# Performance work log

Measured on AMD Instinct MI355X. Metric: run time of the kernel, lower is better.

## Reference

```python
import jax, jax.numpy as jnp
import numpy as np

B, N, E = 4, 8192, 1024
H, G = 16, 64            # num_heads, num_groups
D = E // H               # head_dim = 64
GS = N // G              # group (block) size = 128


def setup_inputs() -> dict:
    key = jax.random.key(0)
    ks = jax.random.split(key, 11)
    std = 0.02
    mk = lambda k, shape: (jax.random.normal(k, shape, dtype=jnp.float32) * std)
    return {
        "q": jax.random.normal(ks[0], (B, N, E), dtype=jnp.float32),
        "k": jax.random.normal(ks[1], (B, N, E), dtype=jnp.float32),
        "v": jax.random.normal(ks[2], (B, N, E), dtype=jnp.float32),
        "Wq": mk(ks[3], (E, E)), "bq": jnp.zeros((E,), jnp.float32),
        "Wk": mk(ks[4], (E, E)), "bk": jnp.zeros((E,), jnp.float32),
        "Wv": mk(ks[5], (E, E)), "bv": jnp.zeros((E,), jnp.float32),
        "Wo": mk(ks[6], (E, E)), "bo": jnp.zeros((E,), jnp.float32),
    }


def reference(q, k, v, Wq, bq, Wk, bk, Wv, bv, Wo, bo):
    b, n, e = q.shape
    scale = 1.0 / (D ** 0.5)

    def proj(x, W, bias):
        # [b,n,e] -> [b,H,G,GS,D]  (split heads, then split seq into groups)
        y = x @ W + bias
        return y.reshape(b, n, H, D).transpose(0, 2, 1, 3).reshape(b, H, G, GS, D)

    qh = proj(q, Wq, bq)
    kh = proj(k, Wk, bk)
    vh = proj(v, Wv, bv)

    # block-diagonal attention: each seq group attends only within itself
    scores = jnp.einsum('bhgqd,bhgkd->bhgqk', qh, kh) * scale  # [b,H,G,GS,GS]
    w = jax.nn.softmax(scores, axis=-1)
    og = jnp.einsum('bhgqk,bhgkd->bhgqd', w, vh)               # [b,H,G,GS,D]

    out = og.reshape(b, H, n, D).transpose(0, 2, 1, 3).reshape(b, n, e)
    out = out @ Wo + bo
    # torch version returns attn_weights of the last group from the loop
    return out, w[:, :, -1]
```

## Files before the change

### kernel.cpp

```cpp
#include <hip/hip_runtime.h>
#include <stdint.h>

#define DEVI static __device__ __forceinline__

typedef __attribute__((ext_vector_type(8))) __bf16 bf16x8;
typedef __attribute__((ext_vector_type(4))) float f32x4;

#define MFMA16(a, b, c) __builtin_amdgcn_mfma_f32_16x16x32_bf16((a), (b), (c), 0, 0, 0)

DEVI uint16_t f2bf(float f) {
  uint32_t u = __builtin_bit_cast(uint32_t, f);
  u += 0x7fffu + ((u >> 16) & 1u);
  return (uint16_t)(u >> 16);
}

DEVI void gload16(const void* g, void* l) {
  __builtin_amdgcn_global_load_lds((const __attribute__((address_space(1))) void*)g,
                                   (__attribute__((address_space(3))) void*)l, 16, 0, 0);
}

#define BARRIER()                         \
  do {                                    \
    __builtin_amdgcn_sched_barrier(0);    \
    __builtin_amdgcn_s_barrier();         \
    __builtin_amdgcn_sched_barrier(0);    \
  } while (0)

__global__ __launch_bounds__(256) void cvt_bf16(const float* __restrict__ in,
                                                uint16_t* __restrict__ out, long n) {
  long i = ((long)blockIdx.x * 256 + threadIdx.x) * 8;
  if (i >= n) return;
  float4 a = *(const float4*)(in + i);
  float4 b = *(const float4*)(in + i + 4);
  union { uint16_t u[8]; uint4 v; } r;
  r.u[0] = f2bf(a.x); r.u[1] = f2bf(a.y); r.u[2] = f2bf(a.z); r.u[3] = f2bf(a.w);
  r.u[4] = f2bf(b.x); r.u[5] = f2bf(b.y); r.u[6] = f2bf(b.z); r.u[7] = f2bf(b.w);
  *(uint4*)(out + i) = r.v;
}

struct W4 {
  const float* W[4];
  uint16_t* Wt[4];
};

__global__ __launch_bounds__(256) void wtrans4(W4 p) {
  __shared__ float t[64][65];
  const float* __restrict__ W = p.W[blockIdx.z];
  uint16_t* __restrict__ Wt = p.Wt[blockIdx.z];
  const int ti = blockIdx.y * 64, tj = blockIdx.x * 64;
  {
    int r = threadIdx.x >> 2, c0 = (threadIdx.x & 3) * 16;
#pragma unroll
    for (int i = 0; i < 16; i += 4) {
      float4 v = *(const float4*)(W + (size_t)(ti + r) * 1024 + tj + c0 + i);
      t[r][c0 + i + 0] = v.x; t[r][c0 + i + 1] = v.y;
      t[r][c0 + i + 2] = v.z; t[r][c0 + i + 3] = v.w;
    }
  }
  __syncthreads();
  {
    int c = threadIdx.x >> 2, r0 = (threadIdx.x & 3) * 16;
    union { uint16_t u[16]; uint4 v[2]; } b;
#pragma unroll
    for (int i = 0; i < 16; ++i) b.u[i] = f2bf(t[r0 + i][c]);
    uint16_t* dst = Wt + (size_t)(tj + c) * 1024 + ti + r0;
    *(uint4*)dst = b.v[0];
    *(uint4*)(dst + 8) = b.v[1];
  }
}

__global__ __launch_bounds__(512, 2) void gemm256(const uint16_t* __restrict__ A,
                                                  const uint16_t* __restrict__ Bt,
                                                  const float* __restrict__ bias,
                                                  void* __restrict__ C, int cf32) {
  __shared__ uint8_t lds[163840];
  const int tid = threadIdx.x;
  const int l = tid & 63, w = tid >> 6;
  const int wr = w >> 2, wc = w & 3;
  const int lc = l & 15, lq = l >> 4;

  const int bid = blockIdx.y * 4 + blockIdx.x;
  const int swz = (bid & 7) * 64 + (bid >> 3);
  const size_t m0 = (size_t)(swz >> 2) * 256;
  const int n0 = (swz & 3) * 256;

  const uint8_t* Ab = (const uint8_t*)A + m0 * 2048;
  const uint8_t* Bb = (const uint8_t*)Bt + (size_t)n0 * 2048;

  const int srow = tid >> 3;
  const int susw = ((tid & 7) ^ (srow & 7)) * 16;

  auto stageA = [&](int sb, int kt) {
#pragma unroll
    for (int j = 0; j < 4; ++j)
      gload16(Ab + (size_t)(j * 64 + srow) * 2048 + kt * 128 + susw,
              lds + sb * 32768 + j * 8192 + w * 1024);
  };
  auto stageB = [&](int db, int kt) {
#pragma unroll
    for (int j = 0; j < 4; ++j)
      gload16(Bb + (size_t)(j * 64 + srow) * 2048 + kt * 128 + susw,
              lds + 98304 + db * 32768 + j * 8192 + w * 1024);
  };

  auto ldsA = [&](int sb, int mi, int kk) -> bf16x8 {
    const int row = wr * 128 + mi * 16 + lc;
    const int u = ((kk * 4 + lq) ^ (row & 7)) * 16;
    return *(const bf16x8*)(lds + sb * 32768 + row * 128 + u);
  };
  auto ldsB = [&](int db, int ni, int kk) -> bf16x8 {
    const int row = wc * 64 + ni * 16 + lc;
    const int u = ((kk * 4 + lq) ^ (row & 7)) * 16;
    return *(const bf16x8*)(lds + 98304 + db * 32768 + row * 128 + u);
  };

  f32x4 acc[8][4] = {};

  stageA(0, 0);
  stageB(0, 0);
  stageA(1, 1);
  asm volatile("s_waitcnt vmcnt(4)" ::: "memory");
  BARRIER();

  for (int t = 0; t < 16; ++t) {
    const int ab = t % 3;
    const int bb = t & 1;
    if (t + 1 < 16) stageB((t + 1) & 1, t + 1);
    if (t + 2 < 16) stageA((t + 2) % 3, t + 2);

#pragma unroll
    for (int kk = 0; kk < 2; ++kk) {
      bf16x8 bF[4], aF[8];
#pragma unroll
      for (int ni = 0; ni < 4; ++ni) bF[ni] = ldsB(bb, ni, kk);
#pragma unroll
      for (int mi = 0; mi < 8; ++mi) aF[mi] = ldsA(ab, mi, kk);
      __builtin_amdgcn_s_setprio(1);
#pragma unroll
      for (int mi = 0; mi < 8; ++mi)
#pragma unroll
        for (int ni = 0; ni < 4; ++ni)
          acc[mi][ni] = MFMA16(aF[mi], bF[ni], acc[mi][ni]);
      __builtin_amdgcn_s_setprio(0);
    }

    if (t < 14)       { asm volatile("s_waitcnt vmcnt(4)" ::: "memory"); }
    else if (t == 14) { asm volatile("s_waitcnt vmcnt(0)" ::: "memory"); }
    if (t < 15) BARRIER();
  }

#pragma unroll
  for (int mi = 0; mi < 8; ++mi) {
#pragma unroll
    for (int ni = 0; ni < 4; ++ni) {
      const int col = n0 + wc * 64 + ni * 16 + lc;
      const float bb2 = bias[col];
#pragma unroll
      for (int r = 0; r < 4; ++r) {
        const size_t row = m0 + wr * 128 + mi * 16 + lq * 4 + r;
        const float vv = acc[mi][ni][r] + bb2;
        if (cf32) ((float*)C)[row * 1024 + col] = vv;
        else      ((uint16_t*)C)[row * 1024 + col] = f2bf(vv);
      }
    }
  }
}

__global__ __launch_bounds__(256) void attn(const uint16_t* __restrict__ Qh,
                                            const uint16_t* __restrict__ Kh,
                                            const uint16_t* __restrict__ Vh,
                                            uint16_t* __restrict__ Oh,
                                            float* __restrict__ Wlast) {
  __shared__ uint16_t Ks[128][72];
  __shared__ uint16_t Vt[64][136];
  __shared__ uint16_t Ps[128][136];

  const int blk = blockIdx.x;
  const int b = blk >> 10;
  const int h = (blk >> 6) & 15;
  const int g = blk & 63;
  const size_t rowbase = (size_t)b * 8192 + (size_t)g * 128;
  const int colbase = h * 64;

  const int tid = threadIdx.x, lane = tid & 63, wv = tid >> 6;
  const int lc = lane & 15, lq = lane >> 4;
  const int m0 = wv * 32;

  {
    const int r = tid >> 1, hf = (tid & 1) * 32;
    const uint16_t* ksrc = Kh + (rowbase + r) * 1024 + colbase + hf;
    const uint16_t* vsrc = Vh + (rowbase + r) * 1024 + colbase + hf;
    union { uint16_t u[32]; uint4 v[4]; } kk, vb;
#pragma unroll
    for (int i = 0; i < 4; ++i) kk.v[i] = *(const uint4*)(ksrc + i * 8);
#pragma unroll
    for (int i = 0; i < 4; ++i) vb.v[i] = *(const uint4*)(vsrc + i * 8);
#pragma unroll
    for (int i = 0; i < 4; ++i) *(uint4*)&Ks[r][hf + i * 8] = kk.v[i];
#pragma unroll
    for (int j = 0; j < 32; ++j) Vt[hf + j][r] = vb.u[j];
  }

  bf16x8 aq[2][2];
#pragma unroll
  for (int mi = 0; mi < 2; ++mi)
#pragma unroll
    for (int ks = 0; ks < 2; ++ks)
      aq[mi][ks] = *(const bf16x8*)(Qh + (rowbase + m0 + mi * 16 + lc) * 1024 +
                                    colbase + ks * 32 + lq * 8);

  __syncthreads();

  f32x4 sacc[2][8] = {};
#pragma unroll
  for (int ks = 0; ks < 2; ++ks) {
#pragma unroll
    for (int ni = 0; ni < 8; ++ni) {
      bf16x8 bk = *(const bf16x8*)&Ks[ni * 16 + lc][ks * 32 + lq * 8];
      sacc[0][ni] = MFMA16(aq[0][ks], bk, sacc[0][ni]);
      sacc[1][ni] = MFMA16(aq[1][ks], bk, sacc[1][ni]);
    }
  }

  const float scale = 0.125f;
  float mx[2][4], sm[2][4];
#pragma unroll
  for (int mi = 0; mi < 2; ++mi)
#pragma unroll
    for (int r = 0; r < 4; ++r) {
      float m = -1e30f;
#pragma unroll
      for (int ni = 0; ni < 8; ++ni) m = fmaxf(m, sacc[mi][ni][r]);
      m = fmaxf(m, __shfl_xor(m, 1));
      m = fmaxf(m, __shfl_xor(m, 2));
      m = fmaxf(m, __shfl_xor(m, 4));
      m = fmaxf(m, __shfl_xor(m, 8));
      mx[mi][r] = m * scale;
    }
#pragma unroll
  for (int mi = 0; mi < 2; ++mi)
#pragma unroll
    for (int ni = 0; ni < 8; ++ni)
#pragma unroll
      for (int r = 0; r < 4; ++r)
        sacc[mi][ni][r] = __expf(sacc[mi][ni][r] * scale - mx[mi][r]);
#pragma unroll
  for (int mi = 0; mi < 2; ++mi)
#pragma unroll
    for (int r = 0; r < 4; ++r) {
      float s = 0.f;
#pragma unroll
      for (int ni = 0; ni < 8; ++ni) s += sacc[mi][ni][r];
      s += __shfl_xor(s, 1); s += __shfl_xor(s, 2);
      s += __shfl_xor(s, 4); s += __shfl_xor(s, 8);
      sm[mi][r] = 1.0f / s;
    }

#pragma unroll
  for (int mi = 0; mi < 2; ++mi)
#pragma unroll
    for (int ni = 0; ni < 8; ++ni)
#pragma unroll
      for (int r = 0; r < 4; ++r) {
        float wgt = sacc[mi][ni][r] * sm[mi][r];
        sacc[mi][ni][r] = wgt;
        Ps[m0 + mi * 16 + lq * 4 + r][ni * 16 + lc] = f2bf(wgt);
      }
  if (g == 63) {
    float* wl = Wlast + (size_t)(b * 16 + h) * 16384;
#pragma unroll
    for (int mi = 0; mi < 2; ++mi)
#pragma unroll
      for (int ni = 0; ni < 8; ++ni)
#pragma unroll
        for (int r = 0; r < 4; ++r)
          wl[(size_t)(m0 + mi * 16 + lq * 4 + r) * 128 + ni * 16 + lc] =
              sacc[mi][ni][r];
  }
  __syncthreads();

  f32x4 oacc[2][4] = {};
#pragma unroll
  for (int ks = 0; ks < 4; ++ks) {
    bf16x8 ap[2], bq[4];
#pragma unroll
    for (int mi = 0; mi < 2; ++mi)
      ap[mi] = *(const bf16x8*)&Ps[m0 + mi * 16 + lc][ks * 32 + lq * 8];
#pragma unroll
    for (int ni = 0; ni < 4; ++ni)
      bq[ni] = *(const bf16x8*)&Vt[ni * 16 + lc][ks * 32 + lq * 8];
#pragma unroll
    for (int mi = 0; mi < 2; ++mi)
#pragma unroll
      for (int ni = 0; ni < 4; ++ni)
        oacc[mi][ni] = MFMA16(ap[mi], bq[ni], oacc[mi][ni]);
  }
#pragma unroll
  for (int mi = 0; mi < 2; ++mi)
#pragma unroll
    for (int ni = 0; ni < 4; ++ni)
#pragma unroll
      for (int r = 0; r < 4; ++r)
        Oh[(rowbase + m0 + mi * 16 + lq * 4 + r) * 1024 + colbase + ni * 16 + lc] =
            f2bf(oacc[mi][ni][r]);
}

extern "C" void kernel_launch(void* const* d_in, const int* in_sizes, int n_in,
                              void* d_out, int out_size, void* d_ws, size_t ws_size,
                              hipStream_t stream) {
  (void)in_sizes; (void)n_in; (void)out_size; (void)ws_size;
  const float* q  = (const float*)d_in[0];
  const float* k  = (const float*)d_in[1];
  const float* v  = (const float*)d_in[2];
  const float* Wq = (const float*)d_in[3];
  const float* bq = (const float*)d_in[4];
  const float* Wk = (const float*)d_in[5];
  const float* bk = (const float*)d_in[6];
  const float* Wv = (const float*)d_in[7];
  const float* bv = (const float*)d_in[8];
  const float* Wo = (const float*)d_in[9];
  const float* bo = (const float*)d_in[10];

  uint8_t* ws = (uint8_t*)d_ws;
  const size_t WSZ = (size_t)1024 * 1024 * 2;
  const size_t TSZ = (size_t)32768 * 1024 * 2;
  uint16_t* Wtq = (uint16_t*)(ws + 0 * WSZ);
  uint16_t* Wtk = (uint16_t*)(ws + 1 * WSZ);
  uint16_t* Wtv = (uint16_t*)(ws + 2 * WSZ);
  uint16_t* Wto = (uint16_t*)(ws + 3 * WSZ);
  uint16_t* Qh  = (uint16_t*)(ws + 4 * WSZ);
  uint16_t* Khp = (uint16_t*)(ws + 4 * WSZ + 1 * TSZ);
  uint16_t* Vhp = (uint16_t*)(ws + 4 * WSZ + 2 * TSZ);
  uint16_t* Xs  = (uint16_t*)(ws + 4 * WSZ + 3 * TSZ);

  W4 wt;
  wt.W[0] = Wq; wt.W[1] = Wk; wt.W[2] = Wv; wt.W[3] = Wo;
  wt.Wt[0] = Wtq; wt.Wt[1] = Wtk; wt.Wt[2] = Wtv; wt.Wt[3] = Wto;
  wtrans4<<<dim3(16, 16, 4), 256, 0, stream>>>(wt);

  const long NE = (long)32768 * 1024;
  const dim3 gg(4, 128), gb(512);
  cvt_bf16<<<16384, 256, 0, stream>>>(q, Xs, NE);
  gemm256<<<gg, gb, 0, stream>>>(Xs, Wtq, bq, Qh, 0);
  cvt_bf16<<<16384, 256, 0, stream>>>(k, Xs, NE);
  gemm256<<<gg, gb, 0, stream>>>(Xs, Wtk, bk, Khp, 0);
  cvt_bf16<<<16384, 256, 0, stream>>>(v, Xs, NE);
  gemm256<<<gg, gb, 0, stream>>>(Xs, Wtv, bv, Vhp, 0);

  float* outp = (float*)d_out;
  attn<<<4096, 256, 0, stream>>>(Qh, Khp, Vhp, Xs, outp + (size_t)32768 * 1024);
  gemm256<<<gg, gb, 0, stream>>>(Xs, Wto, bo, outp, 1);
}
```

Baseline: 473.9 us.

## Fuse fp32-to-bf16 input conversion into a batched QKV projection GEMM

Drops the three separate fp32-to-bf16 conversion kernels and has a new GEMM load fp32 activations straight into registers, convert them and write them to swizzled LDS. The Q, K and V projections are batched into one launch over grid z=3, so there are fewer launches and a larger wave of blocks. This removes one write and one read of a bf16 staging copy for each input. In exchange, the A operand goes through registers with a full vmcnt(0) wait each iteration, so the pipelining may be less deep than in the original gemm256.

```diff
diff --git a/kernel.cpp b/kernel.cpp
--- a/kernel.cpp
+++ b/kernel.cpp
@@ -25,18 +25,6 @@
     __builtin_amdgcn_s_barrier();         \
     __builtin_amdgcn_sched_barrier(0);    \
   } while (0)
-
-__global__ __launch_bounds__(256) void cvt_bf16(const float* __restrict__ in,
-                                                uint16_t* __restrict__ out, long n) {
-  long i = ((long)blockIdx.x * 256 + threadIdx.x) * 8;
-  if (i >= n) return;
-  float4 a = *(const float4*)(in + i);
-  float4 b = *(const float4*)(in + i + 4);
-  union { uint16_t u[8]; uint4 v; } r;
-  r.u[0] = f2bf(a.x); r.u[1] = f2bf(a.y); r.u[2] = f2bf(a.z); r.u[3] = f2bf(a.w);
-  r.u[4] = f2bf(b.x); r.u[5] = f2bf(b.y); r.u[6] = f2bf(b.z); r.u[7] = f2bf(b.w);
-  *(uint4*)(out + i) = r.v;
-}
 
 struct W4 {
   const float* W[4];
@@ -161,6 +149,131 @@
         const float vv = acc[mi][ni][r] + bb2;
         if (cf32) ((float*)C)[row * 1024 + col] = vv;
         else      ((uint16_t*)C)[row * 1024 + col] = f2bf(vv);
+      }
+    }
+  }
+}
+
+struct Proj3 {
+  const float* A[3];
+  const uint16_t* W[3];
+  const float* b[3];
+  uint16_t* C[3];
+};
+
+__global__ __launch_bounds__(512, 2) void gemm_proj3(Proj3 p) {
+  __shared__ uint8_t lds[131072];
+  const int tid = threadIdx.x;
+  const int l = tid & 63, w = tid >> 6;
+  const int wr = w >> 2, wc = w & 3;
+  const int lc = l & 15, lq = l >> 4;
+  const int z = blockIdx.z;
+
+  const int bid = blockIdx.y * 4 + blockIdx.x;
+  const int swz = (bid & 7) * 64 + (bid >> 3);
+  const size_t m0 = (size_t)(swz >> 2) * 256;
+  const int n0 = (swz & 3) * 256;
+
+  const float* Af = p.A[z];
+  const uint8_t* Bb = (const uint8_t*)p.W[z] + (size_t)n0 * 2048;
+  const float* bias = p.b[z];
+  uint16_t* C = p.C[z];
+
+  const int srow = tid >> 3;
+  const int susw = ((tid & 7) ^ (srow & 7)) * 16;
+  auto stageB = [&](int db, int kt) {
+#pragma unroll
+    for (int j = 0; j < 4; ++j)
+      gload16(Bb + (size_t)(j * 64 + srow) * 2048 + kt * 128 + susw,
+              lds + 65536 + db * 32768 + j * 8192 + w * 1024);
+  };
+
+  auto loadA = [&](int kt, float4 (&ra)[8]) {
+#pragma unroll
+    for (int j = 0; j < 8; ++j) {
+      const int row = w * 32 + j * 4 + (l >> 4);
+      ra[j] = *(const float4*)(Af + (m0 + row) * 1024 + kt * 64 + (l & 15) * 4);
+    }
+  };
+  auto writeA = [&](int sel, const float4 (&ra)[8]) {
+#pragma unroll
+    for (int j = 0; j < 8; ++j) {
+      const int row = w * 32 + j * 4 + (l >> 4);
+      const int u = (l & 15) >> 1;
+      union { uint16_t h[4]; uint2 v; } tv;
+      tv.h[0] = f2bf(ra[j].x); tv.h[1] = f2bf(ra[j].y);
+      tv.h[2] = f2bf(ra[j].z); tv.h[3] = f2bf(ra[j].w);
+      *(uint2*)(lds + sel * 32768 + row * 128 + ((u ^ (row & 7)) << 4) + (l & 1) * 8) = tv.v;
+    }
+  };
+
+  auto ldsA = [&](int sb, int mi, int kk) -> bf16x8 {
+    const int row = wr * 128 + mi * 16 + lc;
+    const int u = ((kk * 4 + lq) ^ (row & 7)) * 16;
+    return *(const bf16x8*)(lds + sb * 32768 + row * 128 + u);
+  };
+  auto ldsB = [&](int db, int ni, int kk) -> bf16x8 {
+    const int row = wc * 64 + ni * 16 + lc;
+    const int u = ((kk * 4 + lq) ^ (row & 7)) * 16;
+    return *(const bf16x8*)(lds + 65536 + db * 32768 + row * 128 + u);
+  };
+
+  f32x4 acc[8][4] = {};
+
+  {
+    float4 r0[8];
+    loadA(0, r0);
+    stageB(0, 0);
+    writeA(0, r0);
+    asm volatile("s_waitcnt vmcnt(0)" ::: "memory");
+    asm volatile("s_waitcnt lgkmcnt(0)" ::: "memory");
+  }
+  BARRIER();
+
+  for (int t = 0; t < 16; ++t) {
+    const int cur = t & 1;
+    const bool more = (t + 1 < 16);
+    float4 ra[8];
+    if (more) {
+      stageB(cur ^ 1, t + 1);
+      loadA(t + 1, ra);
+    }
+    __builtin_amdgcn_sched_barrier(0);
+
+#pragma unroll
+    for (int kk = 0; kk < 2; ++kk) {
+      bf16x8 bF[4], aF[8];
+#pragma unroll
+      for (int ni = 0; ni < 4; ++ni) bF[ni] = ldsB(cur, ni, kk);
+#pragma unroll
+      for (int mi = 0; mi < 8; ++mi) aF[mi] = ldsA(cur, mi, kk);
+      __builtin_amdgcn_s_setprio(1);
+#pragma unroll
+      for (int mi = 0; mi < 8; ++mi)
+#pragma unroll
+        for (int ni = 0; ni < 4; ++ni)
+          acc[mi][ni] = MFMA16(aF[mi], bF[ni], acc[mi][ni]);
+      __builtin_amdgcn_s_setprio(0);
+    }
+
+    if (more) {
+      writeA(cur ^ 1, ra);
+      asm volatile("s_waitcnt vmcnt(0)" ::: "memory");
+      asm volatile("s_waitcnt lgkmcnt(0)" ::: "memory");
+      BARRIER();
+    }
+  }
+
+#pragma unroll
+  for (int mi = 0; mi < 8; ++mi) {
+#pragma unroll
+    for (int ni = 0; ni < 4; ++ni) {
+      const int col = n0 + wc * 64 + ni * 16 + lc;
+      const float bb2 = bias[col];
+#pragma unroll
+      for (int r = 0; r < 4; ++r) {
+        const size_t row = m0 + wr * 128 + mi * 16 + lq * 4 + r;
+        C[row * 1024 + col] = f2bf(acc[mi][ni][r] + bb2);
       }
     }
   }
@@ -338,16 +451,14 @@
   wt.Wt[0] = Wtq; wt.Wt[1] = Wtk; wt.Wt[2] = Wtv; wt.Wt[3] = Wto;
   wtrans4<<<dim3(16, 16, 4), 256, 0, stream>>>(wt);
 
-  const long NE = (long)32768 * 1024;
-  const dim3 gg(4, 128), gb(512);
-  cvt_bf16<<<16384, 256, 0, stream>>>(q, Xs, NE);
-  gemm256<<<gg, gb, 0, stream>>>(Xs, Wtq, bq, Qh, 0);
-  cvt_bf16<<<16384, 256, 0, stream>>>(k, Xs, NE);
-  gemm256<<<gg, gb, 0, stream>>>(Xs, Wtk, bk, Khp, 0);
-  cvt_bf16<<<16384, 256, 0, stream>>>(v, Xs, NE);
-  gemm256<<<gg, gb, 0, stream>>>(Xs, Wtv, bv, Vhp, 0);
+  Proj3 p;
+  p.A[0] = q;  p.A[1] = k;  p.A[2] = v;
+  p.W[0] = Wtq; p.W[1] = Wtk; p.W[2] = Wtv;
+  p.b[0] = bq; p.b[1] = bk; p.b[2] = bv;
+  p.C[0] = Qh; p.C[1] = Khp; p.C[2] = Vhp;
+  gemm_proj3<<<dim3(4, 128, 3), 512, 0, stream>>>(p);
 
   float* outp = (float*)d_out;
   attn<<<4096, 256, 0, stream>>>(Qh, Khp, Vhp, Xs, outp + (size_t)32768 * 1024);
-  gemm256<<<gg, gb, 0, stream>>>(Xs, Wto, bo, outp, 1);
-}
+  gemm256<<<dim3(4, 128), 512, 0, stream>>>(Xs, Wto, bo, outp, 1);
+}
```

New measurement: 479.5 us. About the same (+1.2%).

## Split GEMM main loop into four interleaved load/MFMA phases with barriers

Applied to the files above, without the earlier changes.

Restructures the projection GEMM inner loop into four quadrant phases, each loading part of the A/B fragments from LDS and issuing half of the global-to-LDS staging before running a quarter of the MFMAs. This aims to overlap LDS reads and global prefetches with matrix math, in the style of a ping-pong schedule. In exchange it adds many workgroup barriers and lgkmcnt fences per k-step, which can serialize waves if the phases don't balance.

```diff
diff --git a/kernel.cpp b/kernel.cpp
--- a/kernel.cpp
+++ b/kernel.cpp
@@ -24,6 +24,12 @@
     __builtin_amdgcn_sched_barrier(0);    \
     __builtin_amdgcn_s_barrier();         \
     __builtin_amdgcn_sched_barrier(0);    \
+  } while (0)
+
+#define LGKM0_FENCE()                                      \
+  do {                                                     \
+    asm volatile("s_waitcnt lgkmcnt(0)" ::: "memory");     \
+    __builtin_amdgcn_sched_barrier(0);                     \
   } while (0)
 
 __global__ __launch_bounds__(256) void cvt_bf16(const float* __restrict__ in,
@@ -90,15 +96,15 @@
   const int srow = tid >> 3;
   const int susw = ((tid & 7) ^ (srow & 7)) * 16;
 
-  auto stageA = [&](int sb, int kt) {
-#pragma unroll
-    for (int j = 0; j < 4; ++j)
+  auto stageA_h = [&](int sb, int kt, int h) {
+#pragma unroll
+    for (int j = 2 * h; j < 2 * h + 2; ++j)
       gload16(Ab + (size_t)(j * 64 + srow) * 2048 + kt * 128 + susw,
               lds + sb * 32768 + j * 8192 + w * 1024);
   };
-  auto stageB = [&](int db, int kt) {
-#pragma unroll
-    for (int j = 0; j < 4; ++j)
+  auto stageB_h = [&](int db, int kt, int h) {
+#pragma unroll
+    for (int j = 2 * h; j < 2 * h + 2; ++j)
       gload16(Bb + (size_t)(j * 64 + srow) * 2048 + kt * 128 + susw,
               lds + 98304 + db * 32768 + j * 8192 + w * 1024);
   };
@@ -116,33 +122,90 @@
 
   f32x4 acc[8][4] = {};
 
-  stageA(0, 0);
-  stageB(0, 0);
-  stageA(1, 1);
+  stageA_h(0, 0, 0); stageA_h(0, 0, 1);
+  stageB_h(0, 0, 0); stageB_h(0, 0, 1);
+  stageA_h(1, 1, 0); stageA_h(1, 1, 1);
   asm volatile("s_waitcnt vmcnt(4)" ::: "memory");
   BARRIER();
 
   for (int t = 0; t < 16; ++t) {
     const int ab = t % 3;
     const int bb = t & 1;
-    if (t + 1 < 16) stageB((t + 1) & 1, t + 1);
-    if (t + 2 < 16) stageA((t + 2) % 3, t + 2);
+    const int nbB = (t + 1) & 1;
+    const int nbA = (t + 2) % 3;
+    const bool stB = (t + 1) < 16;
+    const bool stA = (t + 2) < 16;
+
+    bf16x8 aF[4][2], bF[4][2], aG[4][2];
 
 #pragma unroll
     for (int kk = 0; kk < 2; ++kk) {
-      bf16x8 bF[4], aF[8];
-#pragma unroll
-      for (int ni = 0; ni < 4; ++ni) bF[ni] = ldsB(bb, ni, kk);
-#pragma unroll
-      for (int mi = 0; mi < 8; ++mi) aF[mi] = ldsA(ab, mi, kk);
-      __builtin_amdgcn_s_setprio(1);
-#pragma unroll
-      for (int mi = 0; mi < 8; ++mi)
-#pragma unroll
-        for (int ni = 0; ni < 4; ++ni)
-          acc[mi][ni] = MFMA16(aF[mi], bF[ni], acc[mi][ni]);
-      __builtin_amdgcn_s_setprio(0);
-    }
+#pragma unroll
+      for (int mi = 0; mi < 4; ++mi) aF[mi][kk] = ldsA(ab, mi, kk);
+#pragma unroll
+      for (int ni = 0; ni < 2; ++ni) bF[ni][kk] = ldsB(bb, ni, kk);
+    }
+    if (stB) stageB_h(nbB, t + 1, 0);
+    BARRIER();
+    LGKM0_FENCE();
+    __builtin_amdgcn_s_setprio(1);
+#pragma unroll
+    for (int mi = 0; mi < 4; ++mi)
+#pragma unroll
+      for (int ni = 0; ni < 2; ++ni) {
+        acc[mi][ni] = MFMA16(aF[mi][0], bF[ni][0], acc[mi][ni]);
+        acc[mi][ni] = MFMA16(aF[mi][1], bF[ni][1], acc[mi][ni]);
+      }
+    __builtin_amdgcn_s_setprio(0);
+    BARRIER();
+
+#pragma unroll
+    for (int kk = 0; kk < 2; ++kk)
+#pragma unroll
+      for (int ni = 2; ni < 4; ++ni) bF[ni][kk] = ldsB(bb, ni, kk);
+    if (stB) stageB_h(nbB, t + 1, 1);
+    BARRIER();
+    LGKM0_FENCE();
+    __builtin_amdgcn_s_setprio(1);
+#pragma unroll
+    for (int mi = 0; mi < 4; ++mi)
+#pragma unroll
+      for (int ni = 2; ni < 4; ++ni) {
+        acc[mi][ni] = MFMA16(aF[mi][0], bF[ni][0], acc[mi][ni]);
+        acc[mi][ni] = MFMA16(aF[mi][1], bF[ni][1], acc[mi][ni]);
+      }
+    __builtin_amdgcn_s_setprio(0);
+    BARRIER();
+
+#pragma unroll
+    for (int kk = 0; kk < 2; ++kk)
+#pragma unroll
+      for (int mi = 0; mi < 4; ++mi) aG[mi][kk] = ldsA(ab, mi + 4, kk);
+    if (stA) stageA_h(nbA, t + 2, 0);
+    BARRIER();
+    LGKM0_FENCE();
+    __builtin_amdgcn_s_setprio(1);
+#pragma unroll
+    for (int mi = 0; mi < 4; ++mi)
+#pragma unroll
+      for (int ni = 0; ni < 2; ++ni) {
+        acc[mi + 4][ni] = MFMA16(aG[mi][0], bF[ni][0], acc[mi + 4][ni]);
+        acc[mi + 4][ni] = MFMA16(aG[mi][1], bF[ni][1], acc[mi + 4][ni]);
+      }
+    __builtin_amdgcn_s_setprio(0);
+    BARRIER();
+
+    if (stA) stageA_h(nbA, t + 2, 1);
+    BARRIER();
+    __builtin_amdgcn_s_setprio(1);
+#pragma unroll
+    for (int mi = 0; mi < 4; ++mi)
+#pragma unroll
+      for (int ni = 2; ni < 4; ++ni) {
+        acc[mi + 4][ni] = MFMA16(aG[mi][0], bF[ni][0], acc[mi + 4][ni]);
+        acc[mi + 4][ni] = MFMA16(aG[mi][1], bF[ni][1], acc[mi + 4][ni]);
+      }
+    __builtin_amdgcn_s_setprio(0);
 
     if (t < 14)       { asm volatile("s_waitcnt vmcnt(4)" ::: "memory"); }
     else if (t == 14) { asm volatile("s_waitcnt vmcnt(0)" ::: "memory"); }
```

After: 471.2 us. Within noise of the previous version (-0.6%).

## Replace 256x256 GEMM tile with 128x128 tile and double-buffered pipeline

Applied to the files above, without the earlier changes.

Swaps the 512-thread 256x256 GEMM (160KB LDS, triple-buffered A, double-buffered B) for a 256-thread 128x128 tile using 48KB LDS, so three blocks can share a CU. B is single-buffered: the B fragments are pulled into registers and a barrier is taken before the next tile is prefetched, while A is double-buffered. The aim is higher occupancy and more blocks to balance the wave across CUs. In exchange each tile has lower arithmetic intensity, generates more global traffic, and adds an extra barrier plus a full vmcnt(0) wait every K step.

```diff
diff --git a/kernel.cpp b/kernel.cpp
--- a/kernel.cpp
+++ b/kernel.cpp
@@ -24,6 +24,12 @@
     __builtin_amdgcn_sched_barrier(0);    \
     __builtin_amdgcn_s_barrier();         \
     __builtin_amdgcn_sched_barrier(0);    \
+  } while (0)
+
+#define LGKM0_FENCE()                                      \
+  do {                                                     \
+    asm volatile("s_waitcnt lgkmcnt(0)" ::: "memory");     \
+    __builtin_amdgcn_sched_barrier(0);                     \
   } while (0)
 
 __global__ __launch_bounds__(256) void cvt_bf16(const float* __restrict__ in,
@@ -69,96 +75,109 @@
   }
 }
 
-__global__ __launch_bounds__(512, 2) void gemm256(const uint16_t* __restrict__ A,
+__global__ __launch_bounds__(256, 3) void gemm128(const uint16_t* __restrict__ A,
                                                   const uint16_t* __restrict__ Bt,
                                                   const float* __restrict__ bias,
                                                   void* __restrict__ C, int cf32) {
-  __shared__ uint8_t lds[163840];
+  __shared__ uint8_t lds[49152];
   const int tid = threadIdx.x;
   const int l = tid & 63, w = tid >> 6;
-  const int wr = w >> 2, wc = w & 3;
+  const int wr = w >> 1, wc = w & 1;
   const int lc = l & 15, lq = l >> 4;
 
-  const int bid = blockIdx.y * 4 + blockIdx.x;
-  const int swz = (bid & 7) * 64 + (bid >> 3);
-  const size_t m0 = (size_t)(swz >> 2) * 256;
-  const int n0 = (swz & 3) * 256;
+  const int bid = blockIdx.y * 8 + blockIdx.x;
+  const int swz = (bid & 7) * 256 + (bid >> 3);
+  const size_t m0 = (size_t)(swz >> 3) * 128;
+  const int n0 = (swz & 7) * 128;
 
   const uint8_t* Ab = (const uint8_t*)A + m0 * 2048;
   const uint8_t* Bb = (const uint8_t*)Bt + (size_t)n0 * 2048;
 
-  const int srow = tid >> 3;
-  const int susw = ((tid & 7) ^ (srow & 7)) * 16;
-
-  auto stageA = [&](int sb, int kt) {
-#pragma unroll
-    for (int j = 0; j < 4; ++j)
-      gload16(Ab + (size_t)(j * 64 + srow) * 2048 + kt * 128 + susw,
-              lds + sb * 32768 + j * 8192 + w * 1024);
+  const int lrow = l >> 3;
+  const int susw = ((l & 7) ^ lrow) * 16;
+
+  auto stageA = [&](int buf, int kt) {
+#pragma unroll
+    for (int j = 0; j < 4; ++j) {
+      const int c = w * 4 + j;
+      gload16(Ab + (size_t)(c * 8 + lrow) * 2048 + kt * 128 + susw,
+              lds + buf * 16384 + c * 1024);
+    }
   };
-  auto stageB = [&](int db, int kt) {
-#pragma unroll
-    for (int j = 0; j < 4; ++j)
-      gload16(Bb + (size_t)(j * 64 + srow) * 2048 + kt * 128 + susw,
-              lds + 98304 + db * 32768 + j * 8192 + w * 1024);
+  auto stageB = [&](int kt) {
+#pragma unroll
+    for (int j = 0; j < 4; ++j) {
+      const int c = w * 4 + j;
+      gload16(Bb + (size_t)(c * 8 + lrow) * 2048 + kt * 128 + susw,
+              lds + 32768 + c * 1024);
+    }
   };
 
-  auto ldsA = [&](int sb, int mi, int kk) -> bf16x8 {
-    const int row = wr * 128 + mi * 16 + lc;
+  auto ldsA = [&](int buf, int mi, int kk) -> bf16x8 {
+    const int row = wr * 64 + mi * 16 + lc;
     const int u = ((kk * 4 + lq) ^ (row & 7)) * 16;
-    return *(const bf16x8*)(lds + sb * 32768 + row * 128 + u);
+    return *(const bf16x8*)(lds + buf * 16384 + row * 128 + u);
   };
-  auto ldsB = [&](int db, int ni, int kk) -> bf16x8 {
+  auto ldsB = [&](int ni, int kk) -> bf16x8 {
     const int row = wc * 64 + ni * 16 + lc;
     const int u = ((kk * 4 + lq) ^ (row & 7)) * 16;
-    return *(const bf16x8*)(lds + 98304 + db * 32768 + row * 128 + u);
+    return *(const bf16x8*)(lds + 32768 + row * 128 + u);
   };
 
-  f32x4 acc[8][4] = {};
+  f32x4 acc[4][4] = {};
 
   stageA(0, 0);
-  stageB(0, 0);
-  stageA(1, 1);
-  asm volatile("s_waitcnt vmcnt(4)" ::: "memory");
+  stageB(0);
+  asm volatile("s_waitcnt vmcnt(0)" ::: "memory");
   BARRIER();
 
   for (int t = 0; t < 16; ++t) {
-    const int ab = t % 3;
-    const int bb = t & 1;
-    if (t + 1 < 16) stageB((t + 1) & 1, t + 1);
-    if (t + 2 < 16) stageA((t + 2) % 3, t + 2);
+    const int cur = t & 1;
+    const bool more = (t + 1 < 16);
+
+    bf16x8 bF[4][2];
+#pragma unroll
+    for (int ni = 0; ni < 4; ++ni)
+#pragma unroll
+      for (int kk = 0; kk < 2; ++kk) bF[ni][kk] = ldsB(ni, kk);
+    LGKM0_FENCE();
+    BARRIER();
+
+    if (more) {
+      stageB(t + 1);
+      stageA(cur ^ 1, t + 1);
+    }
 
 #pragma unroll
     for (int kk = 0; kk < 2; ++kk) {
-      bf16x8 bF[4], aF[8];
-#pragma unroll
-      for (int ni = 0; ni < 4; ++ni) bF[ni] = ldsB(bb, ni, kk);
-#pragma unroll
-      for (int mi = 0; mi < 8; ++mi) aF[mi] = ldsA(ab, mi, kk);
+      bf16x8 aF[4];
+#pragma unroll
+      for (int mi = 0; mi < 4; ++mi) aF[mi] = ldsA(cur, mi, kk);
       __builtin_amdgcn_s_setprio(1);
 #pragma unroll
-      for (int mi = 0; mi < 8; ++mi)
+      for (int mi = 0; mi < 4; ++mi)
 #pragma unroll
         for (int ni = 0; ni < 4; ++ni)
-          acc[mi][ni] = MFMA16(aF[mi], bF[ni], acc[mi][ni]);
+          acc[mi][ni] = MFMA16(aF[mi], bF[ni][kk], acc[mi][ni]);
       __builtin_amdgcn_s_setprio(0);
     }
 
-    if (t < 14)       { asm volatile("s_waitcnt vmcnt(4)" ::: "memory"); }
-    else if (t == 14) { asm volatile("s_waitcnt vmcnt(0)" ::: "memory"); }
-    if (t < 15) BARRIER();
-  }
-
-#pragma unroll
-  for (int mi = 0; mi < 8; ++mi) {
+    if (more) {
+      asm volatile("s_waitcnt vmcnt(0)" ::: "memory");
+      BARRIER();
+    }
+  }
+
+#pragma unroll
+  for (int mi = 0; mi < 4; ++mi) {
 #pragma unroll
     for (int ni = 0; ni < 4; ++ni) {
       const int col = n0 + wc * 64 + ni * 16 + lc;
-      const float bb2 = bias[col];
+      const float bb = bias[col];
 #pragma unroll
       for (int r = 0; r < 4; ++r) {
-        const size_t row = m0 + wr * 128 + mi * 16 + lq * 4 + r;
-        const float vv = acc[mi][ni][r] + bb2;
+        const size_t row = m0 + wr * 64 + mi * 16 + lq * 4 + r;
+        const float vv = acc[mi][ni][r] + bb;
         if (cf32) ((float*)C)[row * 1024 + col] = vv;
         else      ((uint16_t*)C)[row * 1024 + col] = f2bf(vv);
       }
@@ -339,15 +358,15 @@
   wtrans4<<<dim3(16, 16, 4), 256, 0, stream>>>(wt);
 
   const long NE = (long)32768 * 1024;
-  const dim3 gg(4, 128), gb(512);
+  const dim3 gg(8, 256), gb(256);
   cvt_bf16<<<16384, 256, 0, stream>>>(q, Xs, NE);
-  gemm256<<<gg, gb, 0, stream>>>(Xs, Wtq, bq, Qh, 0);
+  gemm128<<<gg, gb, 0, stream>>>(Xs, Wtq, bq, Qh, 0);
   cvt_bf16<<<16384, 256, 0, stream>>>(k, Xs, NE);
-  gemm256<<<gg, gb, 0, stream>>>(Xs, Wtk, bk, Khp, 0);
+  gemm128<<<gg, gb, 0, stream>>>(Xs, Wtk, bk, Khp, 0);
   cvt_bf16<<<16384, 256, 0, stream>>>(v, Xs, NE);
-  gemm256<<<gg, gb, 0, stream>>>(Xs, Wtv, bv, Vhp, 0);
+  gemm128<<<gg, gb, 0, stream>>>(Xs, Wtv, bv, Vhp, 0);
 
   float* outp = (float*)d_out;
   attn<<<4096, 256, 0, stream>>>(Qh, Khp, Vhp, Xs, outp + (size_t)32768 * 1024);
-  gemm256<<<gg, gb, 0, stream>>>(Xs, Wto, bo, outp, 1);
-}
+  gemm128<<<gg, gb, 0, stream>>>(Xs, Wto, bo, outp, 1);
+}
```

Result: no change. 467.7 us (median of 2 runs) (-1.3%).
